# Performance work log

Hardware: AMD Instinct MI355X
Metric: run time of the kernel (lower is better)

Reference implementation:

```python
import jax, jax.numpy as jnp
import numpy as np

EPS = 1e-9
LN_EPS = 1e-5

def _ln(t, g, b):
    m = t.mean(-1, keepdims=True)
    v = ((t - m) ** 2).mean(-1, keepdims=True)
    return (t - m) / jnp.sqrt(v + LN_EPS) * g + b

def _dwconv(t, w, b):
    # t: (B,S,H), w: (H,1,4) depthwise. torch pads 3 on both sides then slices [:S],
    # which equals causal left-pad of 3.
    y = jax.lax.conv_general_dilated(
        t.transpose(0, 2, 1), w, window_strides=(1,), padding=[(3, 0)],
        feature_group_count=w.shape[0], dimension_numbers=("NCH", "OIH", "NCH"))
    return y.transpose(0, 2, 1) + b

def _forward(x, Wq, Wk, Wv, Wo, Wg, We1, We2, Wd1, Wd2, Wa1, Wa2,
             conv_w, conv_b, qn_g, qn_b, kn_g, kn_b, mW1, mb1, mW2, mb2, chunk_size):
    B, S, D = x.shape
    H = Wk.shape[1]
    M = mW1.shape[0]
    q = x @ Wq; k = x @ Wk; v = x @ Wv
    eta = jax.nn.softplus((x @ We1) @ We2)
    delta = jax.nn.softplus((x @ Wd1) @ Wd2)
    alpha = jax.nn.sigmoid((x @ Wa1) @ Wa2)
    q = _ln(_dwconv(q, conv_w, conv_b), qn_g, qn_b)  # computed but unused downstream, as in source
    k = _ln(_dwconv(k, conv_w, conv_b), kn_g, kn_b)
    v = _dwconv(v, conv_w, conv_b)
    n = S // chunk_size
    chunk = lambda t: t.reshape(B, n, chunk_size, H).transpose(1, 0, 2, 3)  # (n,B,C,H)
    xs = (chunk(k), chunk(v), chunk(eta), chunk(delta), chunk(alpha))
    state0 = (jnp.broadcast_to(mW1, (B, M, H)), jnp.broadcast_to(mb1, (B, M)),
              jnp.broadcast_to(mW2, (B, H, M)), jnp.broadcast_to(mb2, (B, H)))

    def step(state, inp):
        W1, b1, W2, b2 = state
        kc, vc, ec, dc, ac = inp  # each (B,C,H)
        inter = jnp.einsum("bch,bmh->bcm", kc, W1) + b1[:, None, :]
        act = jax.nn.gelu(inter, approximate=False)
        out = jnp.einsum("bcm,bhm->bch", act, W2) + b2[:, None, :]
        err = out - vc
        en = jnp.sqrt(jnp.sum(err * err, axis=-1, keepdims=True))  # (B,C,1)
        grad = jnp.where(en > dc, dc * err / (en + EPS), err)
        aw = ac[:, -1, :].mean(-1)[:, None, None]
        ew = ec[:, -1, :].mean(-1)[:, None, None]
        us = grad.mean(1, keepdims=True)   # (B,1,H)
        am = act.mean(1, keepdims=True)    # (B,1,M)
        W1g = jnp.einsum("bom,boh->bmh", am, us)
        W2g = jnp.einsum("boh,bom->bhm", us, am)
        nW1 = aw * W1 - ew * W1g
        nW2 = aw * W2 - ew * W2g
        ab = ac[:, -1, :]; eb = ec[:, -1, :]
        b2u = grad.mean(1)
        b1u = jnp.einsum("bch,bhm->bcm", grad, nW2).mean(1)
        nb2 = ab * b2 - eb * b2u
        nb1 = ab.mean(-1, keepdims=True) * b1 - eb.mean(-1, keepdims=True) * b1u
        # torch updates state under no_grad -> detach
        new_state = jax.tree_util.tree_map(jax.lax.stop_gradient, (nW1, nb1, nW2, nb2))
        return new_state, out

    _, outs = jax.lax.scan(step, state0, xs)  # (n,B,C,H)
    combined = outs.transpose(1, 0, 2, 3).reshape(B, S, H)
    return (combined @ Wo) * jax.nn.sigmoid(x @ Wg)

def setup_inputs():
    key = jax.random.key(0)
    B, S, D, H, M, R = 4, 4096, 1024, 128, 256, 64
    ks = jax.random.split(key, 23)
    g = lambda i, shp, s: jax.random.normal(ks[i], shp, jnp.float32) * s
    return {
        "x": g(0, (B, S, D), 1.0),
        "Wq": g(1, (D, H), 0.02), "Wk": g(2, (D, H), 0.02), "Wv": g(3, (D, H), 0.02),
        "Wo": g(4, (H, D), 0.02), "Wg": g(5, (D, D), 0.02),
        "We1": g(6, (D, R), 0.02), "We2": g(7, (R, H), 0.02),
        "Wd1": g(8, (D, R), 0.02), "Wd2": g(9, (R, H), 0.02),
        "Wa1": g(10, (D, R), 0.02), "Wa2": g(11, (R, H), 0.02),
        "conv_w": g(12, (H, 1, 4), 0.2), "conv_b": g(13, (H,), 0.02),
        "qn_g": jnp.ones((H,), jnp.float32), "qn_b": jnp.zeros((H,), jnp.float32),
        "kn_g": jnp.ones((H,), jnp.float32), "kn_b": jnp.zeros((H,), jnp.float32),
        "mW1": g(14, (M, H), 0.05), "mb1": g(15, (M,), 0.02),
        "mW2": g(16, (H, M), 0.05), "mb2": g(17, (H,), 0.02),
        "chunk_size": 64,
    }

def reference(x, Wq, Wk, Wv, Wo, Wg, We1, We2, Wd1, Wd2, Wa1, Wa2,
              conv_w, conv_b, qn_g, qn_b, kn_g, kn_b, mW1, mb1, mW2, mb2, chunk_size):
    return _forward(x, Wq, Wk, Wv, Wo, Wg, We1, We2, Wd1, Wd2, Wa1, Wa2,
                    conv_w, conv_b, qn_g, qn_b, kn_g, kn_b, mW1, mb1, mW2, mb2, chunk_size)
```

## Files before the change

### kernel.cpp

```cpp
#include <hip/hip_runtime.h>
#include <math.h>

#define Bq 4
#define Sq 4096
#define Dq 1024
#define Hq 128
#define Mq 256
#define Rq 64
#define Cq 64
#define NCHUNK 64
#define BSq (Bq*Sq)

typedef __attribute__((ext_vector_type(8))) short short8;
typedef __attribute__((ext_vector_type(4))) float f32x4;
typedef __attribute__((ext_vector_type(2))) unsigned int uintx2;

#define U_WKVTH  ((size_t)0)
#define U_WKVTL  (U_WKVTH + (size_t)2*Hq*Dq)
#define U_WEDATH (U_WKVTL + (size_t)2*Hq*Dq)
#define U_WEDATL (U_WEDATH + (size_t)3*Rq*Dq)
#define U_WGTH   (U_WEDATL + (size_t)3*Rq*Dq)
#define U_WGTL   (U_WGTH + (size_t)Dq*Dq)
#define U_WE2TH  (U_WGTL + (size_t)Dq*Dq)
#define U_WE2TL  (U_WE2TH + (size_t)Hq*Rq)
#define U_WD2TH  (U_WE2TL + (size_t)Hq*Rq)
#define U_WD2TL  (U_WD2TH + (size_t)Hq*Rq)
#define U_WA2TH  (U_WD2TL + (size_t)Hq*Rq)
#define U_WA2TL  (U_WA2TH + (size_t)Hq*Rq)
#define U_WOTH   (U_WA2TL + (size_t)Hq*Rq)
#define U_WOTL   (U_WOTH + (size_t)Dq*Hq)
#define U_END    (U_WOTL + (size_t)Dq*Hq)

__device__ __forceinline__ float softplusf_(float x){
  return fmaxf(x,0.f) + log1pf(expf(-fabsf(x)));
}
__device__ __forceinline__ float sigmoidf_(float x){
  return 1.f/(1.f+__expf(-x));
}
__device__ __forceinline__ unsigned short bf16rn(float x){
  unsigned u = __float_as_uint(x);
  u += 0x7fffu + ((u>>16)&1u);
  return (unsigned short)(u>>16);
}
__device__ __forceinline__ float bf16tof(unsigned short s){
  return __uint_as_float(((unsigned)s)<<16);
}
__device__ __forceinline__ unsigned cvt_pk_bf16(float a, float b){
  unsigned r;
  asm("v_cvt_pk_bf16_f32 %0, %1, %2" : "=v"(r) : "v"(a), "v"(b));
  return r;
}
__device__ __forceinline__ float lo16f(unsigned p){ return __uint_as_float(p<<16); }
__device__ __forceinline__ float hi16f(unsigned p){ return __uint_as_float(p & 0xffff0000u); }
union pk8 { unsigned u[4]; short8 s; };

__device__ __forceinline__ void g2lds16(const unsigned short* g, void* lds){
  __builtin_amdgcn_global_load_lds(
      (const __attribute__((address_space(1))) unsigned int*)(const void*)g,
      (__attribute__((address_space(3))) unsigned int*)lds,
      16, 0, 0);
}

__device__ __forceinline__ float gelu_fast(float x){
  float z  = x*0.70710678118f;
  float az = fabsf(z);
  float t  = __builtin_amdgcn_rcpf(fmaf(0.3275911f, az, 1.f));
  float p  = fmaf(t, 1.061405429f, -1.453152027f);
  p = fmaf(t, p, 1.421413741f);
  p = fmaf(t, p, -0.284496736f);
  p = fmaf(t, p, 0.254829592f);
  p = p*t;
  float e  = __expf(-az*az);
  float er = copysignf(1.f - p*e, z);
  return 0.5f*x*(1.f + er);
}

template<int BN, int ACT>
__global__ __launch_bounds__(256) void gemm_bf3(
    const float* __restrict__ Af,
    const unsigned short* __restrict__ BhT, const unsigned short* __restrict__ BlT,
    float* __restrict__ C, const float* __restrict__ gate, int N, int K)
{
  constexpr int BM = 128;
  constexpr int PK = 40;
  constexpr int TN = BN/32;
  __shared__ __align__(16) unsigned short As[2][BM*PK];
  __shared__ __align__(16) unsigned short Bs[2][BN*PK];
  const int tid = threadIdx.x;
  const int bm = blockIdx.y*BM, bn = blockIdx.x*BN;
  const int wv = tid>>6, lane = tid&63;
  const int n16 = lane&15, q = lane>>4;
  const int wm = wv>>1, wn = wv&1;

  f32x4 acc[4][TN];
  #pragma unroll
  for (int i=0;i<4;i++){
    #pragma unroll
    for (int j=0;j<TN;j++){ f32x4 z={0.f,0.f,0.f,0.f}; acc[i][j]=z; }
  }
  for (int k0=0;k0<K;k0+=32){
    #pragma unroll
    for (int c0=0;c0<BM*8;c0+=256){
      int c = c0 + tid;
      int row = c>>3, kg = (c&7)*4;
      float4 v = *(const float4*)&Af[(size_t)(bm+row)*K + k0+kg];
      unsigned hp0 = cvt_pk_bf16(v.x, v.y), hp1 = cvt_pk_bf16(v.z, v.w);
      unsigned lp0 = cvt_pk_bf16(v.x-lo16f(hp0), v.y-hi16f(hp0));
      unsigned lp1 = cvt_pk_bf16(v.z-lo16f(hp1), v.w-hi16f(hp1));
      int off = row*PK+kg;
      uintx2 th = {hp0, hp1}, tl = {lp0, lp1};
      *(uintx2*)&As[0][off] = th;
      *(uintx2*)&As[1][off] = tl;
    }
    #pragma unroll
    for (int c0=0;c0<BN*4;c0+=256){
      int c = c0 + tid;
      int row = c>>2, kg = (c&3)*8;
      *(short8*)&Bs[0][row*PK+kg] = *(const short8*)&BhT[(size_t)(bn+row)*K + k0+kg];
      *(short8*)&Bs[1][row*PK+kg] = *(const short8*)&BlT[(size_t)(bn+row)*K + k0+kg];
    }
    __syncthreads();
    short8 a_h[4], a_l[4], b_h[TN], b_l[TN];
    #pragma unroll
    for (int i=0;i<4;i++){
      int r = wm*64 + i*16 + n16;
      a_h[i] = *(const short8*)&As[0][r*PK + q*8];
      a_l[i] = *(const short8*)&As[1][r*PK + q*8];
    }
    #pragma unroll
    for (int j=0;j<TN;j++){
      int r = wn*(BN/2) + j*16 + n16;
      b_h[j] = *(const short8*)&Bs[0][r*PK + q*8];
      b_l[j] = *(const short8*)&Bs[1][r*PK + q*8];
    }
    #pragma unroll
    for (int i=0;i<4;i++){
      #pragma unroll
      for (int j=0;j<TN;j++){
        acc[i][j] = __builtin_amdgcn_mfma_f32_16x16x32_bf16(a_h[i], b_h[j], acc[i][j], 0,0,0);
        acc[i][j] = __builtin_amdgcn_mfma_f32_16x16x32_bf16(a_l[i], b_h[j], acc[i][j], 0,0,0);
        acc[i][j] = __builtin_amdgcn_mfma_f32_16x16x32_bf16(a_h[i], b_l[j], acc[i][j], 0,0,0);
      }
    }
    __syncthreads();
  }
  #pragma unroll
  for (int i=0;i<4;i++){
    #pragma unroll
    for (int j=0;j<TN;j++){
      #pragma unroll
      for (int r=0;r<4;r++){
        int row = bm + wm*64 + i*16 + q*4 + r;
        int col = bn + wn*(BN/2) + j*16 + n16;
        float v = acc[i][j][r];
        if (ACT==1) v = softplusf_(v);
        else if (ACT==2) v = sigmoidf_(v);
        else if (ACT==3) v *= sigmoidf_(gate[(size_t)row*N+col]);
        C[(size_t)row*N+col] = v;
      }
    }
  }
}

template<int BN>
__global__ __launch_bounds__(256) void gemm_bb(
    const unsigned short* __restrict__ Ah, const unsigned short* __restrict__ Al,
    const unsigned short* __restrict__ BhT, const unsigned short* __restrict__ BlT,
    float* __restrict__ C0, float* __restrict__ C1, float* __restrict__ C2, int K)
{
  constexpr int BM = 64;
  constexpr int PK = 40;
  constexpr int TN = BN/32;
  __shared__ __align__(16) unsigned short As[2][BM*PK];
  __shared__ __align__(16) unsigned short Bs[2][BN*PK];
  const int tid = threadIdx.x;
  const int bx = blockIdx.x;
  const int bm = blockIdx.y*BM;
  const int bnB = bx*BN;
  float* __restrict__ C = (bx==0) ? C0 : ((bx==1) ? C1 : C2);
  const int wv = tid>>6, lane = tid&63;
  const int n16 = lane&15, q = lane>>4;
  const int wm = wv>>1, wn = wv&1;

  f32x4 acc[2][TN];
  #pragma unroll
  for (int i=0;i<2;i++){
    #pragma unroll
    for (int j=0;j<TN;j++){ f32x4 z={0.f,0.f,0.f,0.f}; acc[i][j]=z; }
  }
  for (int k0=0;k0<K;k0+=32){
    {
      int row = tid>>2, kg = (tid&3)*8;
      *(short8*)&As[0][row*PK+kg] = *(const short8*)&Ah[(size_t)(bm+row)*K + k0+kg];
      *(short8*)&As[1][row*PK+kg] = *(const short8*)&Al[(size_t)(bm+row)*K + k0+kg];
    }
    #pragma unroll
    for (int c0=0;c0<BN*4;c0+=256){
      int c = c0 + tid;
      int row = c>>2, kg = (c&3)*8;
      *(short8*)&Bs[0][row*PK+kg] = *(const short8*)&BhT[(size_t)(bnB+row)*K + k0+kg];
      *(short8*)&Bs[1][row*PK+kg] = *(const short8*)&BlT[(size_t)(bnB+row)*K + k0+kg];
    }
    __syncthreads();
    short8 a_h[2], a_l[2], b_h[TN], b_l[TN];
    #pragma unroll
    for (int i=0;i<2;i++){
      int r = wm*32 + i*16 + n16;
      a_h[i] = *(const short8*)&As[0][r*PK + q*8];
      a_l[i] = *(const short8*)&As[1][r*PK + q*8];
    }
    #pragma unroll
    for (int j=0;j<TN;j++){
      int r = wn*(BN/2) + j*16 + n16;
      b_h[j] = *(const short8*)&Bs[0][r*PK + q*8];
      b_l[j] = *(const short8*)&Bs[1][r*PK + q*8];
    }
    #pragma unroll
    for (int i=0;i<2;i++){
      #pragma unroll
      for (int j=0;j<TN;j++){
        acc[i][j] = __builtin_amdgcn_mfma_f32_16x16x32_bf16(a_h[i], b_h[j], acc[i][j], 0,0,0);
        acc[i][j] = __builtin_amdgcn_mfma_f32_16x16x32_bf16(a_l[i], b_h[j], acc[i][j], 0,0,0);
        acc[i][j] = __builtin_amdgcn_mfma_f32_16x16x32_bf16(a_h[i], b_l[j], acc[i][j], 0,0,0);
      }
    }
    __syncthreads();
  }
  #pragma unroll
  for (int i=0;i<2;i++){
    #pragma unroll
    for (int j=0;j<TN;j++){
      #pragma unroll
      for (int r=0;r<4;r++){
        int row = bm + wm*32 + i*16 + q*4 + r;
        int col = wn*(BN/2) + j*16 + n16;
        C[(size_t)row*BN+col] = acc[i][j][r];
      }
    }
  }
}

__global__ __launch_bounds__(256) void gemm_eda2(
    const float* __restrict__ te, const float* __restrict__ td, const float* __restrict__ ta,
    const unsigned short* __restrict__ usb,
    float* __restrict__ etab, float* __restrict__ deltab, float* __restrict__ alphab)
{
  constexpr int BM = 64, PK = 40, BN = 128, TN = 4, K = Rq, N = Hq;
  __shared__ __align__(16) unsigned short As[2][BM*PK];
  __shared__ __align__(16) unsigned short Bs[2][BN*PK];
  const int tid = threadIdx.x;
  const int bx = blockIdx.x;
  const int bm = blockIdx.y*BM;
  const float* __restrict__ Af = (bx==0) ? te : (bx==1) ? td : ta;
  const unsigned short* __restrict__ BhT = usb + ((bx==0) ? U_WE2TH : (bx==1) ? U_WD2TH : U_WA2TH);
  const unsigned short* __restrict__ BlT = usb + ((bx==0) ? U_WE2TL : (bx==1) ? U_WD2TL : U_WA2TL);
  float* __restrict__ C = (bx==0) ? etab : (bx==1) ? deltab : alphab;
  const int wv = tid>>6, lane = tid&63;
  const int n16 = lane&15, q = lane>>4;
  const int wm = wv>>1, wn = wv&1;

  f32x4 acc[2][TN];
  #pragma unroll
  for (int i=0;i<2;i++){
    #pragma unroll
    for (int j=0;j<TN;j++){ f32x4 z={0.f,0.f,0.f,0.f}; acc[i][j]=z; }
  }
  for (int k0=0;k0<K;k0+=32){
    #pragma unroll
    for (int c0=0;c0<BM*8;c0+=256){
      int c = c0 + tid;
      int row = c>>3, kg = (c&7)*4;
      float4 v = *(const float4*)&Af[(size_t)(bm+row)*K + k0+kg];
      unsigned hp0 = cvt_pk_bf16(v.x, v.y), hp1 = cvt_pk_bf16(v.z, v.w);
      unsigned lp0 = cvt_pk_bf16(v.x-lo16f(hp0), v.y-hi16f(hp0));
      unsigned lp1 = cvt_pk_bf16(v.z-lo16f(hp1), v.w-hi16f(hp1));
      int off = row*PK+kg;
      uintx2 th = {hp0, hp1}, tl = {lp0, lp1};
      *(uintx2*)&As[0][off] = th;
      *(uintx2*)&As[1][off] = tl;
    }
    #pragma unroll
    for (int c0=0;c0<BN*4;c0+=256){
      int c = c0 + tid;
      int row = c>>2, kg = (c&3)*8;
      *(short8*)&Bs[0][row*PK+kg] = *(const short8*)&BhT[(size_t)row*K + k0+kg];
      *(short8*)&Bs[1][row*PK+kg] = *(const short8*)&BlT[(size_t)row*K + k0+kg];
    }
    __syncthreads();
    short8 a_h[2], a_l[2], b_h[TN], b_l[TN];
    #pragma unroll
    for (int i=0;i<2;i++){
      int r = wm*32 + i*16 + n16;
      a_h[i] = *(const short8*)&As[0][r*PK + q*8];
      a_l[i] = *(const short8*)&As[1][r*PK + q*8];
    }
    #pragma unroll
    for (int j=0;j<TN;j++){
      int r = wn*(BN/2) + j*16 + n16;
      b_h[j] = *(const short8*)&Bs[0][r*PK + q*8];
      b_l[j] = *(const short8*)&Bs[1][r*PK + q*8];
    }
    #pragma unroll
    for (int i=0;i<2;i++){
      #pragma unroll
      for (int j=0;j<TN;j++){
        acc[i][j] = __builtin_amdgcn_mfma_f32_16x16x32_bf16(a_h[i], b_h[j], acc[i][j], 0,0,0);
        acc[i][j] = __builtin_amdgcn_mfma_f32_16x16x32_bf16(a_l[i], b_h[j], acc[i][j], 0,0,0);
        acc[i][j] = __builtin_amdgcn_mfma_f32_16x16x32_bf16(a_h[i], b_l[j], acc[i][j], 0,0,0);
      }
    }
    __syncthreads();
  }
  #pragma unroll
  for (int i=0;i<2;i++){
    #pragma unroll
    for (int j=0;j<TN;j++){
      #pragma unroll
      for (int r=0;r<4;r++){
        int row = bm + wm*32 + i*16 + q*4 + r;
        int col = wn*(BN/2) + j*16 + n16;
        float v = acc[i][j][r];
        v = (bx==2) ? sigmoidf_(v) : softplusf_(v);
        C[(size_t)row*N+col] = v;
      }
    }
  }
}

__global__ __launch_bounds__(256) void splitT_all(
    const float* __restrict__ Wk,  const float* __restrict__ Wv,
    const float* __restrict__ We1, const float* __restrict__ Wd1,
    const float* __restrict__ Wa1, const float* __restrict__ Wg,
    const float* __restrict__ We2, const float* __restrict__ Wd2,
    const float* __restrict__ Wa2, const float* __restrict__ Wo,
    unsigned short* __restrict__ usb)
{
  size_t idx = (size_t)blockIdx.x*256 + threadIdx.x;
#define SEG(SRC, DH, DL, K_, N_) \
  { size_t sz = (size_t)(K_)*(N_); \
    if (idx < sz){ \
      int nn = (int)(idx/(K_)); int k = (int)(idx - (size_t)nn*(K_)); \
      float v = (SRC)[(size_t)k*(N_) + nn]; \
      unsigned short hh = bf16rn(v); \
      (DH)[idx] = hh; (DL)[idx] = bf16rn(v - bf16tof(hh)); \
      return; } \
    idx -= sz; }
  SEG(Wk,  usb+U_WKVTH,                    usb+U_WKVTL,                    Dq, Hq)
  SEG(Wv,  usb+U_WKVTH+(size_t)Hq*Dq,      usb+U_WKVTL+(size_t)Hq*Dq,      Dq, Hq)
  SEG(We1, usb+U_WEDATH,                   usb+U_WEDATL,                   Dq, Rq)
  SEG(Wd1, usb+U_WEDATH+(size_t)Rq*Dq,     usb+U_WEDATL+(size_t)Rq*Dq,     Dq, Rq)
  SEG(Wa1, usb+U_WEDATH+(size_t)2*Rq*Dq,   usb+U_WEDATL+(size_t)2*Rq*Dq,   Dq, Rq)
  SEG(Wg,  usb+U_WGTH,                     usb+U_WGTL,                     Dq, Dq)
  SEG(We2, usb+U_WE2TH,                    usb+U_WE2TL,                    Rq, Hq)
  SEG(Wd2, usb+U_WD2TH,                    usb+U_WD2TL,                    Rq, Hq)
  SEG(Wa2, usb+U_WA2TH,                    usb+U_WA2TL,                    Rq, Hq)
  SEG(Wo,  usb+U_WOTH,                     usb+U_WOTL,                     Hq, Dq)
#undef SEG
}

__global__ __launch_bounds__(256) void splitX(const float* __restrict__ A,
    unsigned short* __restrict__ h, unsigned short* __restrict__ l)
{
  size_t idx = ((size_t)blockIdx.x*256 + threadIdx.x)*4;
  float4 v = *(const float4*)&A[idx];
  unsigned hp0 = cvt_pk_bf16(v.x, v.y), hp1 = cvt_pk_bf16(v.z, v.w);
  unsigned lp0 = cvt_pk_bf16(v.x-lo16f(hp0), v.y-hi16f(hp0));
  unsigned lp1 = cvt_pk_bf16(v.z-lo16f(hp1), v.w-hi16f(hp1));
  uintx2 th = {hp0, hp1}, tl = {lp0, lp1};
  *(uintx2*)&h[idx] = th;
  *(uintx2*)&l[idx] = tl;
}

__global__ __launch_bounds__(128) void conv_ln_kernel(
  const float* __restrict__ k_raw, const float* __restrict__ v_raw,
  const float* __restrict__ conv_w, const float* __restrict__ conv_b,
  const float* __restrict__ kn_g, const float* __restrict__ kn_b,
  unsigned short* __restrict__ khi, unsigned short* __restrict__ klo,
  float* __restrict__ v_out)
{
  int s = blockIdx.x, b = blockIdx.y, which = blockIdx.z;
  int h = threadIdx.x;
  const float* src = (which==0) ? k_raw : v_raw;
  float acc = conv_b[h];
  #pragma unroll
  for (int j=0;j<4;j++){
    int ss = s-3+j;
    if (ss>=0) acc += conv_w[h*4+j]*src[((size_t)b*Sq+ss)*Hq + h];
  }
  if (which==0){
    __shared__ float red[4];
    float sv = acc, s2 = acc*acc;
    #pragma unroll
    for (int off=32; off>0; off>>=1){
      sv += __shfl_down(sv, off, 64);
      s2 += __shfl_down(s2, off, 64);
    }
    if ((h&63)==0){ red[(h>>6)*2]=sv; red[(h>>6)*2+1]=s2; }
    __syncthreads();
    float mean = (red[0]+red[2])*(1.f/128.f);
    float var  = (red[1]+red[3])*(1.f/128.f) - mean*mean;
    float y = (acc-mean)*rsqrtf(var+1e-5f)*kn_g[h]+kn_b[h];
    unsigned short hh = bf16rn(y);
    size_t idx = ((size_t)b*Sq+s)*Hq + h;
    khi[idx] = hh;
    klo[idx] = bf16rn(y - bf16tof(hh));
  } else {
    v_out[((size_t)b*Sq+s)*Hq + h] = acc;
  }
}

#define OFF_KCH   0
#define OFF_KCL   16384
#define OFF_ACTH  32768
#define OFF_SAM   65536
#define OFF_SUS   66560
#define OFF_PEN   67072
#define OFF_DRED  70144
#define OFF_SUU   78336
#define OFF_SAB   78368
#define OFF_SEB   78880
#define OFF_SABP  79392
#define OFF_SEBP  79400
#define LDS_TOTAL 79408

__global__ __launch_bounds__(512, 2) void fused_scan_wg(
  const unsigned short* __restrict__ khi, const unsigned short* __restrict__ klo,
  const float* __restrict__ v_c,
  const float* __restrict__ eta, const float* __restrict__ delta,
  const float* __restrict__ alpha,
  const float* __restrict__ mW1, const float* __restrict__ mb1,
  const float* __restrict__ mW2, const float* __restrict__ mb2,
  float* __restrict__ combined,
  const float* __restrict__ x,
  const unsigned short* __restrict__ WgTh, const unsigned short* __restrict__ WgTl,
  float* __restrict__ glog)
{
  __shared__ __align__(16) char smem[LDS_TOTAL];
  const int blk = blockIdx.x;
  const int tid = threadIdx.x;
  const int wv = tid >> 6;
  const int lane = tid & 63;
  const int n = lane & 15;
  const int q = lane >> 4;

  if (blk >= 4){
    unsigned short* As_h = (unsigned short*)smem;
    unsigned short* As_l = As_h + 128*40;
    unsigned short* Bs_h = As_l + 128*40;
    unsigned short* Bs_l = Bs_h + 128*40;
    const int g = blk - 4;
    const int bm = (g>>3)*128, bn = (g&7)*128;
    const int wm = wv&3, wn = wv>>2;
    f32x4 acc[2][4];
    #pragma unroll
    for (int i=0;i<2;i++){
      #pragma unroll
      for (int j=0;j<4;j++){ f32x4 z={0.f,0.f,0.f,0.f}; acc[i][j]=z; }
    }
    for (int k0=0;k0<Dq;k0+=32){
      #pragma unroll
      for (int r=0;r<2;r++){
        int idx = tid + 512*r;
        int row = idx>>3, kg = (idx&7)*4;
        float4 v = *(const float4*)&x[(size_t)(bm+row)*Dq + k0+kg];
        unsigned hp0 = cvt_pk_bf16(v.x, v.y), hp1 = cvt_pk_bf16(v.z, v.w);
        unsigned lp0 = cvt_pk_bf16(v.x-lo16f(hp0), v.y-hi16f(hp0));
        unsigned lp1 = cvt_pk_bf16(v.z-lo16f(hp1), v.w-hi16f(hp1));
        int off = row*40+kg;
        uintx2 th = {hp0, hp1}, tl = {lp0, lp1};
        *(uintx2*)&As_h[off] = th;
        *(uintx2*)&As_l[off] = tl;
      }
      {
        int row = tid>>2, kg = (tid&3)*8;
        *(short8*)&Bs_h[row*40+kg] = *(const short8*)&WgTh[(size_t)(bn+row)*Dq + k0+kg];
        *(short8*)&Bs_l[row*40+kg] = *(const short8*)&WgTl[(size_t)(bn+row)*Dq + k0+kg];
      }
      __syncthreads();
      short8 a_h[2], a_l[2], b_h[4], b_l[4];
      #pragma unroll
      for (int i=0;i<2;i++){
        int r = wm*32 + i*16 + n;
        a_h[i] = *(const short8*)&As_h[r*40 + q*8];
        a_l[i] = *(const short8*)&As_l[r*40 + q*8];
      }
      #pragma unroll
      for (int j=0;j<4;j++){
        int r = wn*64 + j*16 + n;
        b_h[j] = *(const short8*)&Bs_h[r*40 + q*8];
        b_l[j] = *(const short8*)&Bs_l[r*40 + q*8];
      }
      #pragma unroll
      for (int i=0;i<2;i++){
        #pragma unroll
        for (int j=0;j<4;j++){
          acc[i][j] = __builtin_amdgcn_mfma_f32_16x16x32_bf16(a_h[i], b_h[j], acc[i][j], 0,0,0);
          acc[i][j] = __builtin_amdgcn_mfma_f32_16x16x32_bf16(a_l[i], b_h[j], acc[i][j], 0,0,0);
          acc[i][j] = __builtin_amdgcn_mfma_f32_16x16x32_bf16(a_h[i], b_l[j], acc[i][j], 0,0,0);
        }
      }
      __syncthreads();
    }
    #pragma unroll
    for (int i=0;i<2;i++){
      #pragma unroll
      for (int j=0;j<4;j++){
        #pragma unroll
        for (int r=0;r<4;r++){
          int row = bm + wm*32 + i*16 + q*4 + r;
          int col = bn + wn*64 + j*16 + n;
          glog[(size_t)row*Dq+col] = acc[i][j][r];
        }
      }
    }
    return;
  }

  unsigned short* kc_hi  = (unsigned short*)(smem + OFF_KCH);
  unsigned short* kc_lo  = (unsigned short*)(smem + OFF_KCL);
  unsigned short* act_hi = (unsigned short*)(smem + OFF_ACTH);
  float* Sam = (float*)(smem + OFF_SAM);
  float* Sus = (float*)(smem + OFF_SUS);
  float* pen = (float*)(smem + OFF_PEN);
  float* Dred= (float*)(smem + OFF_DRED);
  float* Suu = (float*)(smem + OFF_SUU);
  float* Sab = (float*)(smem + OFF_SAB);
  float* Seb = (float*)(smem + OFF_SEB);
  float* Sabp = (float*)(smem + OFF_SABP);
  float* Sebp = (float*)(smem + OFF_SEBP);

  const int b = blk;
  const int h = wv*16 + n;
  float w1m[2][4][8];
  float w2m[8][8];
  float b1reg[2];
  float b2n[4];
  #pragma unroll
  for (int tt=0;tt<2;tt++){
    int m = (2*wv+tt)*16 + n;
    #pragma unroll
    for (int ks=0;ks<4;ks++){
      const float* p = mW1 + (size_t)m*Hq + ks*32 + q*8;
      #pragma unroll
      for (int j=0;j<8;j++) w1m[tt][ks][j] = p[j];
    }
    b1reg[tt] = mb1[m];
  }
  {
    #pragma unroll
    for (int ks2=0;ks2<8;ks2++){
      const float* p = mW2 + (size_t)h*Mq + ks2*32 + q*8;
      #pragma unroll
      for (int j=0;j<8;j++) w2m[ks2][j] = p[j];
    }
    #pragma unroll
    for (int r=0;r<4;r++) b2n[r] = mb2[wv*16 + q*4 + r];
  }
  float aw = 0.f, ew = 0.f;
  float am_own[2] = {0.f, 0.f};

  const unsigned short* khb = khi + (size_t)b*Sq*Hq;
  const unsigned short* klb = klo + (size_t)b*Sq*Hq;

  const int c0s = (wv*2+0)*4 + (lane>>4);
  const int c1s = (wv*2+1)*4 + (lane>>4);
  const int soff0 = c0s*Hq + ((((lane&15)^(c0s&15)))<<3);
  const int soff1 = c1s*Hq + ((((lane&15)^(c1s&15)))<<3);
  char* d_kh0 = smem + OFF_KCH + (wv*2+0)*1024;
  char* d_kh1 = smem + OFF_KCH + (wv*2+1)*1024;
  char* d_kl0 = smem + OFF_KCL + (wv*2+0)*1024;
  char* d_kl1 = smem + OFF_KCL + (wv*2+1)*1024;
  g2lds16(khb + soff0, d_kh0);
  g2lds16(khb + soff1, d_kh1);
  g2lds16(klb + soff0, d_kl0);
  g2lds16(klb + soff1, d_kl1);

  for (int t=0; t<NCHUNK; ++t){
    const size_t base = ((size_t)b*Sq + (size_t)t*Cq)*Hq;
    __syncthreads();

    f32x4 vvv[4], ddd[4];
    #pragma unroll
    for (int ct=0;ct<4;ct++){
      size_t off = base + (size_t)(ct*16+n)*Hq + wv*16 + q*4;
      vvv[ct] = *(const f32x4*)&v_c[off];
      ddd[ct] = *(const f32x4*)&delta[off];
    }
    float ab_=0.f, eb_=0.f;
    if (tid < 128){
      ab_ = alpha[base + 63*Hq + tid];
      eb_ = eta[base + 63*Hq + tid];
    }

    if (t > 0){
      float4 s0[4], s1[4];
      #pragma unroll
      for (int ks=0;ks<4;ks++){
        s0[ks] = *(const float4*)&Sus[ks*32 + q*8];
        s1[ks] = *(const float4*)&Sus[ks*32 + q*8 + 4];
      }
      float4 u0 = *(const float4*)&Suu[0];
      float4 u1 = *(const float4*)&Suu[4];
      float uu = u0.x+u0.y+u0.z+u0.w+u1.x+u1.y+u1.z+u1.w;
      #pragma unroll
      for (int tt=0;tt<2;tt++){
        int m = (2*wv+tt)*16 + n;
        float amm = am_own[tt];
        float eam = ew*amm;
        #pragma unroll
        for (int ks=0;ks<4;ks++){
          #pragma unroll
          for (int j=0;j<4;j++){
            w1m[tt][ks][j]   = aw*w1m[tt][ks][j]   - eam*s0[ks][j];
            w1m[tt][ks][j+4] = aw*w1m[tt][ks][j+4] - eam*s1[ks][j];
          }
        }
        float dsum = 0.f;
        #pragma unroll
        for (int w8=0;w8<8;w8++) dsum += Dred[w8*256 + m];
        b1reg[tt] = aw*b1reg[tt] - ew*(aw*dsum - ew*uu*amm);
      }
    }

    f32x4 acc1[2][4];
    #pragma unroll
    for (int tt=0;tt<2;tt++){
      #pragma unroll
      for (int ct=0;ct<4;ct++){ f32x4 z={0.f,0.f,0.f,0.f}; acc1[tt][ct]=z; }
    }
    __builtin_amdgcn_s_setprio(1);
    #pragma unroll
    for (int ks=0;ks<4;ks++){
      pk8 BH[2], BL[2];
      #pragma unroll
      for (int tt=0;tt<2;tt++){
        #pragma unroll
        for (int jp=0;jp<4;jp++){
          float a0 = w1m[tt][ks][2*jp], a1 = w1m[tt][ks][2*jp+1];
          unsigned hp = cvt_pk_bf16(a0, a1);
          BH[tt].u[jp] = hp;
          BL[tt].u[jp] = cvt_pk_bf16(a0 - lo16f(hp), a1 - hi16f(hp));
        }
      }
      #pragma unroll
      for (int ct=0;ct<4;ct++){
        int c = ct*16 + n;
        int off = c*Hq + ((((ks*4+q)^n))<<3);
        short8 ah = *(const short8*)&kc_hi[off];
        short8 al = *(const short8*)&kc_lo[off];
        #pragma unroll
        for (int tt=0;tt<2;tt++){
          acc1[tt][ct] = __builtin_amdgcn_mfma_f32_16x16x32_bf16(ah, BH[tt].s, acc1[tt][ct], 0,0,0);
          acc1[tt][ct] = __builtin_amdgcn_mfma_f32_16x16x32_bf16(al, BH[tt].s, acc1[tt][ct], 0,0,0);
          acc1[tt][ct] = __builtin_amdgcn_mfma_f32_16x16x32_bf16(ah, BL[tt].s, acc1[tt][ct], 0,0,0);
        }
      }
    }
    __builtin_amdgcn_s_setprio(0);
    #pragma unroll
    for (int tt=0;tt<2;tt++){
      int m = (2*wv+tt)*16 + n;
      float b1v = b1reg[tt];
      float amsum = 0.f;
      #pragma unroll
      for (int ct=0;ct<4;ct++){
        #pragma unroll
        for (int r=0;r<4;r++){
          float g = gelu_fast(acc1[tt][ct][r] + b1v);
          amsum += g;
          int c = ct*16 + q*4 + r;
          int pg = (m>>3) ^ (c & 15);
          act_hi[c*Mq + (pg<<3) + (m&7)] = bf16rn(g);
        }
      }
      amsum += __shfl_xor(amsum, 16, 64);
      amsum += __shfl_xor(amsum, 32, 64);
      am_own[tt] = amsum*(1.f/64.f);
      if (q==0) Sam[m] = am_own[tt];
    }
    if (tid < 128){ Sab[tid] = ab_; Seb[tid] = eb_; }
    if (wv < 2){
      float a2 = ab_, e2 = eb_;
      #pragma unroll
      for (int mk=1;mk<64;mk<<=1){ a2 += __shfl_xor(a2,mk,64); e2 += __shfl_xor(e2,mk,64); }
      if (lane==0){ Sabp[wv] = a2; Sebp[wv] = e2; }
    }
    __syncthreads();

    aw = (Sabp[0]+Sabp[1])*(1.f/128.f);
    ew = (Sebp[0]+Sebp[1])*(1.f/128.f);

    {
      const size_t nb = (size_t)((t+1<NCHUNK)?(t+1):t)*Cq*Hq;
      g2lds16(khb + nb + soff0, d_kh0);
      g2lds16(khb + nb + soff1, d_kh1);
      g2lds16(klb + nb + soff0, d_kl0);
      g2lds16(klb + nb + soff1, d_kl1);
    }

    f32x4 acc2[4];
    #pragma unroll
    for (int ct=0;ct<4;ct++){ f32x4 z={0.f,0.f,0.f,0.f}; acc2[ct]=z; }
    __builtin_amdgcn_s_setprio(1);
    #pragma unroll
    for (int ks2=0;ks2<8;ks2++){
      pk8 BH, BL;
      #pragma unroll
      for (int jp=0;jp<4;jp++){
        float a0 = w2m[ks2][2*jp], a1 = w2m[ks2][2*jp+1];
        unsigned hp = cvt_pk_bf16(a0, a1);
        BH.u[jp] = hp;
        BL.u[jp] = cvt_pk_bf16(a0 - lo16f(hp), a1 - hi16f(hp));
      }
      #pragma unroll
      for (int ct=0;ct<4;ct++){
        int c = ct*16 + n;
        int off = c*Mq + ((((ks2*4+q)^n))<<3);
        short8 ah = *(const short8*)&act_hi[off];
        acc2[ct] = __builtin_amdgcn_mfma_f32_16x16x32_bf16(BH.s, ah, acc2[ct], 0,0,0);
        acc2[ct] = __builtin_amdgcn_mfma_f32_16x16x32_bf16(BL.s, ah, acc2[ct], 0,0,0);
      }
    }
    __builtin_amdgcn_s_setprio(0);

    float err[4][4];
    {
      float* cb = combined + base;
      #pragma unroll
      for (int ct=0;ct<4;ct++){
        int c = ct*16 + n;
        f32x4 ov;
        #pragma unroll
        for (int r=0;r<4;r++){
          float o = acc2[ct][r] + b2n[r];
          ov[r] = o;
          err[ct][r] = o - vvv[ct][r];
        }
        *(f32x4*)&cb[(size_t)c*Hq + wv*16 + q*4] = ov;
      }
      #pragma unroll
      for (int ct=0;ct<4;ct++){
        float s = err[ct][0]*err[ct][0] + err[ct][1]*err[ct][1]
                + err[ct][2]*err[ct][2] + err[ct][3]*err[ct][3];
        s += __shfl_xor(s, 16, 64);
        s += __shfl_xor(s, 32, 64);
        if (q==0) pen[(ct*16+n)*12 + wv] = s;
      }
    }
    __syncthreads();

    float en_c[4];
    #pragma unroll
    for (int ct=0;ct<4;ct++){
      int c = ct*16 + n;
      float4 e0 = *(const float4*)&pen[c*12];
      float4 e1 = *(const float4*)&pen[c*12+4];
      en_c[ct] = sqrtf(e0.x+e0.y+e0.z+e0.w+e1.x+e1.y+e1.z+e1.w);
    }
    float us_r[4];
    #pragma unroll
    for (int r=0;r<4;r++){
      float s = 0.f;
      #pragma unroll
      for (int ct=0;ct<4;ct++){
        float e = err[ct][r];
        float dvv = ddd[ct][r];
        float en = en_c[ct];
        float g = (en > dvv) ? dvv*e*__builtin_amdgcn_rcpf(en+1e-9f) : e;
        s += g;
      }
      s += __shfl_xor(s,1,64); s += __shfl_xor(s,2,64);
      s += __shfl_xor(s,4,64); s += __shfl_xor(s,8,64);
      us_r[r] = s*(1.f/64.f);
    }
    if (n==0){
      #pragma unroll
      for (int r=0;r<4;r++) Sus[wv*16 + q*4 + r] = us_r[r];
    }
    {
      float uun = us_r[0]*us_r[0] + us_r[1]*us_r[1]
                + us_r[2]*us_r[2] + us_r[3]*us_r[3];
      uun += __shfl_xor(uun, 16, 64);
      uun += __shfl_xor(uun, 32, 64);
      if (lane==0) Suu[wv] = uun;
    }
    {
      f32x4 sab = *(const f32x4*)&Sab[wv*16 + q*4];
      f32x4 seb = *(const f32x4*)&Seb[wv*16 + q*4];
      #pragma unroll
      for (int r=0;r<4;r++) b2n[r] = sab[r]*b2n[r] - seb[r]*us_r[r];
    }
    float ush;
    {
      int src = (n>>2)<<4;
      float p0 = __shfl(us_r[0], src, 64);
      float p1 = __shfl(us_r[1], src, 64);
      float p2 = __shfl(us_r[2], src, 64);
      float p3 = __shfl(us_r[3], src, 64);
      int rr = n&3;
      ush = (rr==0) ? p0 : (rr==1) ? p1 : (rr==2) ? p2 : p3;
    }

    {
      const bool bb0 = (n&1);
      float p1[8][4];
      #pragma unroll
      for (int k2=0;k2<8;k2++){
        #pragma unroll
        for (int l=0;l<4;l++){
          float mine = ush * (bb0 ? w2m[k2][l+4] : w2m[k2][l]);
          float oth  = ush * (bb0 ? w2m[k2][l]   : w2m[k2][l+4]);
          p1[k2][l] = mine + __shfl_xor(oth, 1, 64);
        }
      }
      const bool bb1 = (n>>1)&1;
      float p2[4][4];
      #pragma unroll
      for (int k2=0;k2<4;k2++){
        #pragma unroll
        for (int l=0;l<4;l++){
          float mine = bb1 ? p1[2*k2+1][l] : p1[2*k2][l];
          float oth  = bb1 ? p1[2*k2][l]   : p1[2*k2+1][l];
          p2[k2][l] = mine + __shfl_xor(oth, 2, 64);
        }
      }
      const bool bb2 = (n>>2)&1;
      float p3[2][4];
      #pragma unroll
      for (int k2=0;k2<2;k2++){
        #pragma unroll
        for (int l=0;l<4;l++){
          float mine = bb2 ? p2[2*k2+1][l] : p2[2*k2][l];
          float oth  = bb2 ? p2[2*k2][l]   : p2[2*k2+1][l];
          p3[k2][l] = mine + __shfl_xor(oth, 4, 64);
        }
      }
      const bool bb3 = (n>>3)&1;
      float4 p4;
      {
        float m0 = bb3 ? p3[1][0] : p3[0][0];
        float o0 = bb3 ? p3[0][0] : p3[1][0];
        p4.x = m0 + __shfl_xor(o0, 8, 64);
        float m1 = bb3 ? p3[1][1] : p3[0][1];
        float o1 = bb3 ? p3[0][1] : p3[1][1];
        p4.y = m1 + __shfl_xor(o1, 8, 64);
        float m2 = bb3 ? p3[1][2] : p3[0][2];
        float o2 = bb3 ? p3[0][2] : p3[1][2];
        p4.z = m2 + __shfl_xor(o2, 8, 64);
        float m3 = bb3 ? p3[1][3] : p3[0][3];
        float o3 = bb3 ? p3[0][3] : p3[1][3];
        p4.w = m3 + __shfl_xor(o3, 8, 64);
      }
      int base_m = (n>>1)*32 + q*8 + (n&1)*4;
      *(float4*)&Dred[wv*256 + base_m] = p4;
    }

    {
      float eus = ew*ush;
      #pragma unroll
      for (int ks2=0;ks2<8;ks2++){
        float4 a0 = *(const float4*)&Sam[ks2*32 + q*8];
        float4 a1 = *(const float4*)&Sam[ks2*32 + q*8 + 4];
        #pragma unroll
        for (int j=0;j<4;j++){
          w2m[ks2][j]   = aw*w2m[ks2][j]   - eus*a0[j];
          w2m[ks2][j+4] = aw*w2m[ks2][j+4] - eus*a1[j];
        }
      }
    }
  }
}

extern "C" void kernel_launch(void* const* d_in, const int* in_sizes, int n_in,
                              void* d_out, int out_size, void* d_ws, size_t ws_size,
                              hipStream_t stream)
{
  const float* x    = (const float*)d_in[0];
  const float* Wk   = (const float*)d_in[2];
  const float* Wv   = (const float*)d_in[3];
  const float* Wo   = (const float*)d_in[4];
  const float* Wg   = (const float*)d_in[5];
  const float* We1  = (const float*)d_in[6];
  const float* We2  = (const float*)d_in[7];
  const float* Wd1  = (const float*)d_in[8];
  const float* Wd2  = (const float*)d_in[9];
  const float* Wa1  = (const float*)d_in[10];
  const float* Wa2  = (const float*)d_in[11];
  const float* conv_w = (const float*)d_in[12];
  const float* conv_b = (const float*)d_in[13];
  const float* kn_g = (const float*)d_in[16];
  const float* kn_b = (const float*)d_in[17];
  const float* mW1  = (const float*)d_in[18];
  const float* mb1  = (const float*)d_in[19];
  const float* mW2  = (const float*)d_in[20];
  const float* mb2  = (const float*)d_in[21];
  float* out = (float*)d_out;

  float* ws = (float*)d_ws;
  size_t o = 0;
  float* k_raw = ws + o; o += (size_t)BSq*Hq;
  float* v_raw = ws + o; o += (size_t)BSq*Hq;
  float* te    = ws + o; o += (size_t)BSq*Rq;
  float* td    = ws + o; o += (size_t)BSq*Rq;
  float* ta    = ws + o; o += (size_t)BSq*Rq;
  float* glog  = ws + o; o += (size_t)BSq*Dq;
  float* etab  = ws + o; o += (size_t)BSq*Hq;
  float* deltab= ws + o; o += (size_t)BSq*Hq;
  float* alphab= ws + o; o += (size_t)BSq*Hq;
  float* kslot = ws + o; o += (size_t)BSq*Hq;
  float* v_c   = ws + o; o += (size_t)BSq*Hq;
  float* comb  = ws + o; o += (size_t)BSq*Hq;
  unsigned short* usb = (unsigned short*)(ws + o);

  unsigned short* khi = (unsigned short*)kslot;
  unsigned short* klo = khi + (size_t)BSq*Hq;

  unsigned short* xh = (unsigned short*)glog;
  unsigned short* xl = xh + (size_t)BSq*Dq;

  {
    size_t total = 2*(size_t)Hq*Dq + 3*(size_t)Rq*Dq + (size_t)Dq*Dq
                 + 3*(size_t)Hq*Rq + (size_t)Dq*Hq;
    splitT_all<<<(unsigned)(total/256), 256, 0, stream>>>(
        Wk, Wv, We1, Wd1, Wa1, Wg, We2, Wd2, Wa2, Wo, usb);
  }
  splitX<<<(size_t)BSq*Dq/4/256, 256, 0, stream>>>(x, xh, xl);

  dim3 blk(256);
  gemm_bb<128><<<dim3(2, BSq/64), blk, 0, stream>>>(xh, xl, usb+U_WKVTH, usb+U_WKVTL, k_raw, v_raw, nullptr, Dq);
  gemm_bb<64> <<<dim3(3, BSq/64), blk, 0, stream>>>(xh, xl, usb+U_WEDATH, usb+U_WEDATL, te, td, ta, Dq);
  gemm_eda2<<<dim3(3, BSq/64), blk, 0, stream>>>(te, td, ta, usb, etab, deltab, alphab);
  conv_ln_kernel<<<dim3(Sq, Bq, 2), dim3(128), 0, stream>>>(
      k_raw, v_raw, conv_w, conv_b, kn_g, kn_b, khi, klo, v_c);
  fused_scan_wg<<<dim3(4 + (BSq/128)*(Dq/128)), dim3(512), 0, stream>>>(
      khi, klo, v_c, etab, deltab, alphab, mW1, mb1, mW2, mb2, comb,
      x, usb+U_WGTH, usb+U_WGTL, glog);
  gemm_bf3<128,3><<<dim3(Dq/128, BSq/128), blk, 0, stream>>>(comb, usb+U_WOTH, usb+U_WOTL, out, glog, Dq, Hq);
}
```

Before: 1.216 ms.

## Fuse x split into projection GEMM and merge k/v/eda projections into one launch

Removes the separate splitX pass and converts x from fp32 to hi/lo bf16 inside the projection GEMM's shared-memory load. The k, v, eta, delta and alpha projections run in a single launch over a concatenated 448-column weight. The last column tile overlaps the previous one by 64 columns and keeps only the alpha half. The conv+layernorm kernel now handles k and v together and two sequence positions per block. This avoids writing and re-reading the bf16 copies of x and cuts launches, at the cost of repeating the fp32-to-bf16 conversion in every column block and some redundant MFMA work in the overlapping tile.

```diff
diff --git a/kernel.cpp b/kernel.cpp
--- a/kernel.cpp
+++ b/kernel.cpp
@@ -15,21 +15,19 @@
 typedef __attribute__((ext_vector_type(4))) float f32x4;
 typedef __attribute__((ext_vector_type(2))) unsigned int uintx2;
 
-#define U_WKVTH  ((size_t)0)
-#define U_WKVTL  (U_WKVTH + (size_t)2*Hq*Dq)
-#define U_WEDATH (U_WKVTL + (size_t)2*Hq*Dq)
-#define U_WEDATL (U_WEDATH + (size_t)3*Rq*Dq)
-#define U_WGTH   (U_WEDATL + (size_t)3*Rq*Dq)
-#define U_WGTL   (U_WGTH + (size_t)Dq*Dq)
-#define U_WE2TH  (U_WGTL + (size_t)Dq*Dq)
-#define U_WE2TL  (U_WE2TH + (size_t)Hq*Rq)
-#define U_WD2TH  (U_WE2TL + (size_t)Hq*Rq)
-#define U_WD2TL  (U_WD2TH + (size_t)Hq*Rq)
-#define U_WA2TH  (U_WD2TL + (size_t)Hq*Rq)
-#define U_WA2TL  (U_WA2TH + (size_t)Hq*Rq)
-#define U_WOTH   (U_WA2TL + (size_t)Hq*Rq)
-#define U_WOTL   (U_WOTH + (size_t)Dq*Hq)
-#define U_END    (U_WOTL + (size_t)Dq*Hq)
+#define U_XPH   ((size_t)0)
+#define U_XPL   (U_XPH + (size_t)448*Dq)
+#define U_WGTH  (U_XPL + (size_t)448*Dq)
+#define U_WGTL  (U_WGTH + (size_t)Dq*Dq)
+#define U_WE2TH (U_WGTL + (size_t)Dq*Dq)
+#define U_WE2TL (U_WE2TH + (size_t)Hq*Rq)
+#define U_WD2TH (U_WE2TL + (size_t)Hq*Rq)
+#define U_WD2TL (U_WD2TH + (size_t)Hq*Rq)
+#define U_WA2TH (U_WD2TL + (size_t)Hq*Rq)
+#define U_WA2TL (U_WA2TH + (size_t)Hq*Rq)
+#define U_WOTH  (U_WA2TL + (size_t)Hq*Rq)
+#define U_WOTL  (U_WOTH + (size_t)Dq*Hq)
+#define U_END   (U_WOTL + (size_t)Dq*Hq)
 
 __device__ __forceinline__ float softplusf_(float x){
   return fmaxf(x,0.f) + log1pf(expf(-fabsf(x)));
@@ -162,22 +160,19 @@
   }
 }
 
-template<int BN>
-__global__ __launch_bounds__(256) void gemm_bb(
-    const unsigned short* __restrict__ Ah, const unsigned short* __restrict__ Al,
+__global__ __launch_bounds__(256) void gemm_xproj(
+    const float* __restrict__ x,
     const unsigned short* __restrict__ BhT, const unsigned short* __restrict__ BlT,
-    float* __restrict__ C0, float* __restrict__ C1, float* __restrict__ C2, int K)
+    float* __restrict__ k_raw, float* __restrict__ v_raw,
+    float* __restrict__ te, float* __restrict__ td, float* __restrict__ ta)
 {
-  constexpr int BM = 64;
-  constexpr int PK = 40;
-  constexpr int TN = BN/32;
+  constexpr int BM = 64, PK = 40, BN = 128, TN = 4, K = Dq;
   __shared__ __align__(16) unsigned short As[2][BM*PK];
   __shared__ __align__(16) unsigned short Bs[2][BN*PK];
   const int tid = threadIdx.x;
   const int bx = blockIdx.x;
   const int bm = blockIdx.y*BM;
-  const int bnB = bx*BN;
-  float* __restrict__ C = (bx==0) ? C0 : ((bx==1) ? C1 : C2);
+  const int bnB = (bx<=2) ? bx*128 : 320;
   const int wv = tid>>6, lane = tid&63;
   const int n16 = lane&15, q = lane>>4;
   const int wm = wv>>1, wn = wv&1;
@@ -189,10 +184,18 @@
     for (int j=0;j<TN;j++){ f32x4 z={0.f,0.f,0.f,0.f}; acc[i][j]=z; }
   }
   for (int k0=0;k0<K;k0+=32){
-    {
-      int row = tid>>2, kg = (tid&3)*8;
-      *(short8*)&As[0][row*PK+kg] = *(const short8*)&Ah[(size_t)(bm+row)*K + k0+kg];
-      *(short8*)&As[1][row*PK+kg] = *(const short8*)&Al[(size_t)(bm+row)*K + k0+kg];
+    #pragma unroll
+    for (int c0=0;c0<BM*8;c0+=256){
+      int c = c0 + tid;
+      int row = c>>3, kg = (c&7)*4;
+      float4 v = *(const float4*)&x[(size_t)(bm+row)*K + k0+kg];
+      unsigned hp0 = cvt_pk_bf16(v.x, v.y), hp1 = cvt_pk_bf16(v.z, v.w);
+      unsigned lp0 = cvt_pk_bf16(v.x-lo16f(hp0), v.y-hi16f(hp0));
+      unsigned lp1 = cvt_pk_bf16(v.z-lo16f(hp1), v.w-hi16f(hp1));
+      int off = row*PK+kg;
+      uintx2 th = {hp0, hp1}, tl = {lp0, lp1};
+      *(uintx2*)&As[0][off] = th;
+      *(uintx2*)&As[1][off] = tl;
     }
     #pragma unroll
     for (int c0=0;c0<BN*4;c0+=256){
@@ -233,8 +236,18 @@
       #pragma unroll
       for (int r=0;r<4;r++){
         int row = bm + wm*32 + i*16 + q*4 + r;
-        int col = wn*(BN/2) + j*16 + n16;
-        C[(size_t)row*BN+col] = acc[i][j][r];
+        int col = wn*64 + j*16 + n16;
+        float v = acc[i][j][r];
+        if (bx==0){
+          k_raw[(size_t)row*Hq + col] = v;
+        } else if (bx==1){
+          v_raw[(size_t)row*Hq + col] = v;
+        } else if (bx==2){
+          if (col < 64) te[(size_t)row*Rq + col] = v;
+          else          td[(size_t)row*Rq + col-64] = v;
+        } else {
+          if (col >= 64) ta[(size_t)row*Rq + col-64] = v;
+        }
       }
     }
   }
@@ -345,68 +358,60 @@
       (DH)[idx] = hh; (DL)[idx] = bf16rn(v - bf16tof(hh)); \
       return; } \
     idx -= sz; }
-  SEG(Wk,  usb+U_WKVTH,                    usb+U_WKVTL,                    Dq, Hq)
-  SEG(Wv,  usb+U_WKVTH+(size_t)Hq*Dq,      usb+U_WKVTL+(size_t)Hq*Dq,      Dq, Hq)
-  SEG(We1, usb+U_WEDATH,                   usb+U_WEDATL,                   Dq, Rq)
-  SEG(Wd1, usb+U_WEDATH+(size_t)Rq*Dq,     usb+U_WEDATL+(size_t)Rq*Dq,     Dq, Rq)
-  SEG(Wa1, usb+U_WEDATH+(size_t)2*Rq*Dq,   usb+U_WEDATL+(size_t)2*Rq*Dq,   Dq, Rq)
-  SEG(Wg,  usb+U_WGTH,                     usb+U_WGTL,                     Dq, Dq)
-  SEG(We2, usb+U_WE2TH,                    usb+U_WE2TL,                    Rq, Hq)
-  SEG(Wd2, usb+U_WD2TH,                    usb+U_WD2TL,                    Rq, Hq)
-  SEG(Wa2, usb+U_WA2TH,                    usb+U_WA2TL,                    Rq, Hq)
-  SEG(Wo,  usb+U_WOTH,                     usb+U_WOTL,                     Hq, Dq)
+  SEG(Wk,  usb+U_XPH,                   usb+U_XPL,                   Dq, Hq)
+  SEG(Wv,  usb+U_XPH+(size_t)128*Dq,    usb+U_XPL+(size_t)128*Dq,    Dq, Hq)
+  SEG(We1, usb+U_XPH+(size_t)256*Dq,    usb+U_XPL+(size_t)256*Dq,    Dq, Rq)
+  SEG(Wd1, usb+U_XPH+(size_t)320*Dq,    usb+U_XPL+(size_t)320*Dq,    Dq, Rq)
+  SEG(Wa1, usb+U_XPH+(size_t)384*Dq,    usb+U_XPL+(size_t)384*Dq,    Dq, Rq)
+  SEG(Wg,  usb+U_WGTH,                  usb+U_WGTL,                  Dq, Dq)
+  SEG(We2, usb+U_WE2TH,                 usb+U_WE2TL,                 Rq, Hq)
+  SEG(Wd2, usb+U_WD2TH,                 usb+U_WD2TL,                 Rq, Hq)
+  SEG(Wa2, usb+U_WA2TH,                 usb+U_WA2TL,                 Rq, Hq)
+  SEG(Wo,  usb+U_WOTH,                  usb+U_WOTL,                  Hq, Dq)
 #undef SEG
 }
 
-__global__ __launch_bounds__(256) void splitX(const float* __restrict__ A,
-    unsigned short* __restrict__ h, unsigned short* __restrict__ l)
-{
-  size_t idx = ((size_t)blockIdx.x*256 + threadIdx.x)*4;
-  float4 v = *(const float4*)&A[idx];
-  unsigned hp0 = cvt_pk_bf16(v.x, v.y), hp1 = cvt_pk_bf16(v.z, v.w);
-  unsigned lp0 = cvt_pk_bf16(v.x-lo16f(hp0), v.y-hi16f(hp0));
-  unsigned lp1 = cvt_pk_bf16(v.z-lo16f(hp1), v.w-hi16f(hp1));
-  uintx2 th = {hp0, hp1}, tl = {lp0, lp1};
-  *(uintx2*)&h[idx] = th;
-  *(uintx2*)&l[idx] = tl;
-}
-
-__global__ __launch_bounds__(128) void conv_ln_kernel(
+__global__ __launch_bounds__(256) void conv_ln_kernel(
   const float* __restrict__ k_raw, const float* __restrict__ v_raw,
   const float* __restrict__ conv_w, const float* __restrict__ conv_b,
   const float* __restrict__ kn_g, const float* __restrict__ kn_b,
   unsigned short* __restrict__ khi, unsigned short* __restrict__ klo,
   float* __restrict__ v_out)
 {
-  int s = blockIdx.x, b = blockIdx.y, which = blockIdx.z;
-  int h = threadIdx.x;
-  const float* src = (which==0) ? k_raw : v_raw;
-  float acc = conv_b[h];
+  const int b  = blockIdx.y;
+  const int sp = threadIdx.x >> 7;
+  const int h  = threadIdx.x & 127;
+  const int s  = blockIdx.x*2 + sp;
+  const int w4 = threadIdx.x >> 6;
+  const float cb = conv_b[h];
+  float acck = cb, accv = cb;
   #pragma unroll
   for (int j=0;j<4;j++){
     int ss = s-3+j;
-    if (ss>=0) acc += conv_w[h*4+j]*src[((size_t)b*Sq+ss)*Hq + h];
-  }
-  if (which==0){
-    __shared__ float red[4];
-    float sv = acc, s2 = acc*acc;
-    #pragma unroll
-    for (int off=32; off>0; off>>=1){
-      sv += __shfl_down(sv, off, 64);
-      s2 += __shfl_down(s2, off, 64);
-    }
-    if ((h&63)==0){ red[(h>>6)*2]=sv; red[(h>>6)*2+1]=s2; }
-    __syncthreads();
-    float mean = (red[0]+red[2])*(1.f/128.f);
-    float var  = (red[1]+red[3])*(1.f/128.f) - mean*mean;
-    float y = (acc-mean)*rsqrtf(var+1e-5f)*kn_g[h]+kn_b[h];
-    unsigned short hh = bf16rn(y);
-    size_t idx = ((size_t)b*Sq+s)*Hq + h;
-    khi[idx] = hh;
-    klo[idx] = bf16rn(y - bf16tof(hh));
-  } else {
-    v_out[((size_t)b*Sq+s)*Hq + h] = acc;
-  }
+    if (ss>=0){
+      float w = conv_w[h*4+j];
+      size_t idx = ((size_t)b*Sq+ss)*Hq + h;
+      acck += w*k_raw[idx];
+      accv += w*v_raw[idx];
+    }
+  }
+  __shared__ float red[8];
+  float sv = acck, s2 = acck*acck;
+  #pragma unroll
+  for (int off=32; off>0; off>>=1){
+    sv += __shfl_down(sv, off, 64);
+    s2 += __shfl_down(s2, off, 64);
+  }
+  if ((threadIdx.x&63)==0){ red[w4*2]=sv; red[w4*2+1]=s2; }
+  __syncthreads();
+  float mean = (red[sp*4+0]+red[sp*4+2])*(1.f/128.f);
+  float var  = (red[sp*4+1]+red[sp*4+3])*(1.f/128.f) - mean*mean;
+  float y = (acck-mean)*rsqrtf(var+1e-5f)*kn_g[h]+kn_b[h];
+  unsigned short hh = bf16rn(y);
+  size_t idx = ((size_t)b*Sq+s)*Hq + h;
+  khi[idx] = hh;
+  klo[idx] = bf16rn(y - bf16tof(hh));
+  v_out[idx] = accv;
 }
 
 #define OFF_KCH   0
@@ -915,22 +920,17 @@
   unsigned short* khi = (unsigned short*)kslot;
   unsigned short* klo = khi + (size_t)BSq*Hq;
 
-  unsigned short* xh = (unsigned short*)glog;
-  unsigned short* xl = xh + (size_t)BSq*Dq;
-
   {
-    size_t total = 2*(size_t)Hq*Dq + 3*(size_t)Rq*Dq + (size_t)Dq*Dq
-                 + 3*(size_t)Hq*Rq + (size_t)Dq*Hq;
+    size_t total = (size_t)448*Dq + (size_t)Dq*Dq + 3*(size_t)Hq*Rq + (size_t)Dq*Hq;
     splitT_all<<<(unsigned)(total/256), 256, 0, stream>>>(
         Wk, Wv, We1, Wd1, Wa1, Wg, We2, Wd2, Wa2, Wo, usb);
   }
-  splitX<<<(size_t)BSq*Dq/4/256, 256, 0, stream>>>(x, xh, xl);
 
   dim3 blk(256);
-  gemm_bb<128><<<dim3(2, BSq/64), blk, 0, stream>>>(xh, xl, usb+U_WKVTH, usb+U_WKVTL, k_raw, v_raw, nullptr, Dq);
-  gemm_bb<64> <<<dim3(3, BSq/64), blk, 0, stream>>>(xh, xl, usb+U_WEDATH, usb+U_WEDATL, te, td, ta, Dq);
+  gemm_xproj<<<dim3(4, BSq/64), blk, 0, stream>>>(
+      x, usb+U_XPH, usb+U_XPL, k_raw, v_raw, te, td, ta);
   gemm_eda2<<<dim3(3, BSq/64), blk, 0, stream>>>(te, td, ta, usb, etab, deltab, alphab);
-  conv_ln_kernel<<<dim3(Sq, Bq, 2), dim3(128), 0, stream>>>(
+  conv_ln_kernel<<<dim3(Sq/2, Bq), dim3(256), 0, stream>>>(
       k_raw, v_raw, conv_w, conv_b, kn_g, kn_b, khi, klo, v_c);
   fused_scan_wg<<<dim3(4 + (BSq/128)*(Dq/128)), dim3(512), 0, stream>>>(
       khi, klo, v_c, etab, deltab, alphab, mW1, mb1, mW2, mb2, comb,
```

Measured after the change: 1.200 ms. No clear change (-1.3%).
